# Performance work log

Hardware: AMD Instinct MI355X
Metric: run time of the kernel (lower is better)

The kernel has to match this reference:

```python
import jax, jax.numpy as jnp
import numpy as np

B, S, D, H = 2, 2048, 512, 8
DK = D // H
MASK_VALUE = -1e9


def setup_inputs() -> dict:
    key = jax.random.key(0)
    ks = jax.random.split(key, 12)
    scale = 1.0 / np.sqrt(D)
    inp = {
        "query": jax.random.normal(ks[0], (B, S, D), jnp.float32),
        "key": jax.random.normal(ks[1], (B, S, D), jnp.float32),
        "value": jax.random.normal(ks[2], (B, S, D), jnp.float32),
        # causal mask, broadcastable over batch and heads
        "mask": jnp.tril(jnp.ones((S, S), jnp.int32))[None, None, :, :],
        "Wq": jax.random.normal(ks[3], (D, D), jnp.float32) * scale,
        "bq": jax.random.normal(ks[4], (D,), jnp.float32) * scale,
        "Wk": jax.random.normal(ks[5], (D, D), jnp.float32) * scale,
        "bk": jax.random.normal(ks[6], (D,), jnp.float32) * scale,
        "Wv": jax.random.normal(ks[7], (D, D), jnp.float32) * scale,
        "bv": jax.random.normal(ks[8], (D,), jnp.float32) * scale,
        "Wo": jax.random.normal(ks[9], (D, D), jnp.float32) * scale,
        "bo": jax.random.normal(ks[10], (D,), jnp.float32) * scale,
    }
    return inp


def reference(query, key, value, mask, Wq, bq, Wk, bk, Wv, bv, Wo, bo):
    # linear projections (torch Linear: x @ W.T + b)
    q = query @ Wq.T + bq
    k = key @ Wk.T + bk
    v = value @ Wv.T + bv
    # split heads: [B,S,D] -> [B,H,S,DK]
    q = q.reshape(B, S, H, DK).transpose(0, 2, 1, 3)
    k = k.reshape(B, S, H, DK).transpose(0, 2, 1, 3)
    v = v.reshape(B, S, H, DK).transpose(0, 2, 1, 3)
    # scaled dot-product attention with explicit [B,H,S,S] score matrix
    scores = jnp.einsum("bhqd,bhkd->bhqk", q, k) / jnp.sqrt(jnp.float32(DK))
    scores = jnp.where(mask == 0, jnp.float32(MASK_VALUE), scores)
    attn = jax.nn.softmax(scores, axis=-1)
    x = jnp.einsum("bhqk,bhkd->bhqd", attn, v)
    # merge heads: [B,H,S,DK] -> [B,S,D]
    x = x.transpose(0, 2, 1, 3).reshape(B, S, D)
    return x @ Wo.T + bo
```

## Files before the change

### kernel.cpp

```cpp
#include <hip/hip_runtime.h>
#include <hip/hip_bf16.h>

#define B_   2
#define S_   2048
#define D_   512
#define H_   8
#define DK_  64
#define M_   (B_*S_)

typedef float  floatx4 __attribute__((ext_vector_type(4)));
typedef __bf16 bf16x8  __attribute__((ext_vector_type(8)));

#define MFMA16x16x32(a,b,c) __builtin_amdgcn_mfma_f32_16x16x32_bf16((a),(b),(c),0,0,0)

static __device__ __forceinline__ void load_lds16(const void* g, void* l) {
  __builtin_amdgcn_global_load_lds(
      (const __attribute__((address_space(1))) void*)g,
      (__attribute__((address_space(3))) void*)l,
      16, 0, 0);
}

static __device__ __forceinline__ bf16x8 cvt8(float4 a, float4 b) {
  bf16x8 r;
  r[0]=(__bf16)a.x; r[1]=(__bf16)a.y; r[2]=(__bf16)a.z; r[3]=(__bf16)a.w;
  r[4]=(__bf16)b.x; r[5]=(__bf16)b.y; r[6]=(__bf16)b.z; r[7]=(__bf16)b.w;
  return r;
}

static __device__ __forceinline__ int part_idx(int bh, int t, int s) {
  const int g = t >> 3;
  const int basec = (g == 2) ? 16 : ((g == 3) ? 40 : 0);
  return bh*72 + basec + (t - 8*g)*(g + 1) + s;
}

__global__ __launch_bounds__(256) void cvt_weights(
    const float* __restrict__ w0, const float* __restrict__ w1,
    const float* __restrict__ w2, const float* __restrict__ w3,
    __bf16* __restrict__ out)
{
  const int idx = (blockIdx.x * 256 + threadIdx.x) * 4;
  const float* src = (idx < 524288) ? ((idx < 262144) ? w0 : w1)
                                    : ((idx < 786432) ? w2 : w3);
  const int off = idx & 0x3FFFF;
  float4 v = *(const float4*)(src + off);
  __bf16* o = out + idx;
  o[0]=(__bf16)v.x; o[1]=(__bf16)v.y; o[2]=(__bf16)v.z; o[3]=(__bf16)v.w;
}


__global__ __launch_bounds__(256) void proj_qkv(
    const float* __restrict__ q_in, const float* __restrict__ k_in,
    const float* __restrict__ v_in, const __bf16* __restrict__ Wball,
    const float* __restrict__ bq, const float* __restrict__ bk, const float* __restrict__ bv,
    __bf16* __restrict__ Qb, __bf16* __restrict__ Kb, __bf16* __restrict__ Vtb)
{
  __shared__ __align__(16) __bf16 smem[12288];

  const int z = blockIdx.z;
  const float*  X32  = (z==0) ? q_in : (z==1) ? k_in : v_in;
  const __bf16* W    = Wball + (size_t)z * (D_*D_);
  const float*  bias = (z==0) ? bq : (z==1) ? bk : bv;

  const int m0 = blockIdx.x * 64;
  const int n0 = blockIdx.y * 128;
  const int tid  = threadIdx.x;
  const int w    = tid >> 6;
  const int lane = tid & 63;
  const int lcol = lane & 15;
  const int quad = lane >> 4;
  const int wm = w & 1, wn = w >> 1;

  const int au  = tid;
  const int arow = au >> 2, ac8 = (au & 3) * 8;
  const float* xsrc = X32 + (size_t)(m0 + arow)*D_ + ac8;

  floatx4 zero = {0.f,0.f,0.f,0.f};
  floatx4 acc[2][4];
#pragma unroll
  for (int i = 0; i < 2; ++i)
#pragma unroll
    for (int nt = 0; nt < 4; ++nt) acc[i][nt] = zero;

  auto stageB = [&](int bsel, int k0) {
#pragma unroll
    for (int j = 0; j < 2; ++j) {
      const int u = (j*4 + w)*64 + lane;
      load_lds16(W + (size_t)(n0 + (u >> 2))*D_ + k0 + (u & 3)*8,
                 (char*)(smem + 4096 + bsel*4096) + (j*4 + w)*1024);
    }
  };

  float4 f0, f1;
  stageB(0, 0);
  f0 = *(const float4*)(xsrc);
  f1 = *(const float4*)(xsrc + 4);
  *(bf16x8*)(smem + au*8) = cvt8(f0, f1);

  for (int it = 0; it < 16; ++it) {
    __syncthreads();
    const bool havenext = (it + 1 < 16);
    float4 g0, g1;
    if (havenext) {
      stageB((it+1)&1, (it+1)*32);
      g0 = *(const float4*)(xsrc + (it+1)*32);
      g1 = *(const float4*)(xsrc + (it+1)*32 + 4);
    }
    const __bf16* ab = smem + (it&1)*2048;
    const __bf16* bb = smem + 4096 + (it&1)*4096;
    bf16x8 af[2], bf[4];
#pragma unroll
    for (int i = 0; i < 2; ++i)
      af[i] = *(const bf16x8*)(ab + (wm*32 + i*16 + lcol)*32 + quad*8);
#pragma unroll
    for (int nt = 0; nt < 4; ++nt)
      bf[nt] = *(const bf16x8*)(bb + (wn*64 + nt*16 + lcol)*32 + quad*8);
#pragma unroll
    for (int i = 0; i < 2; ++i)
#pragma unroll
      for (int nt = 0; nt < 4; ++nt)
        acc[i][nt] = MFMA16x16x32(af[i], bf[nt], acc[i][nt]);
    if (havenext)
      *(bf16x8*)(smem + ((it+1)&1)*2048 + au*8) = cvt8(g0, g1);
  }

  __syncthreads();
#pragma unroll
  for (int nt = 0; nt < 4; ++nt) {
    const int n = n0 + wn*64 + nt*16 + lcol;
    const float bias_n = bias[n];
    const int h_l = (n >> 6) & 1;
    const int dk  = n & 63;
#pragma unroll
    for (int i = 0; i < 2; ++i)
#pragma unroll
      for (int r = 0; r < 4; ++r) {
        const int m = m0 + wm*32 + i*16 + quad*4 + r;
        const float val = acc[i][nt][r] + bias_n;
        const int klo = m & 63;
        int off;
        if (z == 0) {
          off = klo*64 + dk;
        } else if (z == 1) {
          off = (((klo>>4)*2 + (dk>>5))*64 + ((dk>>3)&3)*16 + (klo&15))*8 + (dk&7);
        } else {
          off = (((dk>>4)*2 + (klo>>5))*64 + ((klo>>3)&3)*16 + (dk&15))*8 + (klo&7);
        }
        smem[h_l*4096 + off] = (__bf16)val;
      }
  }
  __syncthreads();

  __bf16* dst = (z==0) ? Qb : (z==1) ? Kb : Vtb;
  const int bb2 = m0 >> 11;
  const int hh0 = n0 >> 6;
  const int cc0 = (m0 & 2047) >> 6;
#pragma unroll
  for (int it2 = 0; it2 < 4; ++it2) {
    const int u = it2*256 + tid;
    const int p = u >> 9, o = u & 511;
    const size_t base = ((size_t)(bb2*H_ + hh0 + p))*(S_*DK_) + (size_t)cc0*4096;
    *(bf16x8*)(dst + base + o*8) = *(const bf16x8*)(smem + p*4096 + o*8);
  }
}

__global__ __launch_bounds__(256) void attn_fwd(
    const __bf16* __restrict__ Qb, const __bf16* __restrict__ Kb,
    const __bf16* __restrict__ Vtb, __bf16* __restrict__ attnb,
    __bf16* __restrict__ Pb, float* __restrict__ Lb)
{
  __shared__ __align__(16) __bf16 kbuf[2][4096];
  __shared__ __align__(16) __bf16 vbuf[2][4096];
  __shared__ __align__(16) __bf16 pbuf[4][16*72];

  const int tid  = threadIdx.x;
  const int w    = tid >> 6;
  const int lane = tid & 63;
  const int lcol = lane & 15;
  const int quad = lane >> 4;
  const int hh = blockIdx.y;
  const int bb = blockIdx.z;

  const int wid = blockIdx.x;
  int t, s;
  if (wid < 8)       { t = wid;                  s = 0; }
  else if (wid < 24) { int u = wid - 8;  t = 8  + (u>>1); s = u & 1; }
  else if (wid < 48) { int u = wid - 24; int q3 = u/3; t = 16 + q3; s = u - 3*q3; }
  else               { int u = wid - 48; t = 24 + (u>>2); s = u & 3; }
  const bool single = (wid < 8);

  const int cbeg = s*8;
  const int cend = (cbeg + 8 < t + 1) ? (cbeg + 8) : (t + 1);
  const int q0  = t * 64;
  const int qr0 = q0 + w*16;

  const __bf16* Qp = Qb  + (size_t)(bb*H_ + hh) * S_ * DK_;
  const __bf16* Kp = Kb  + (size_t)(bb*H_ + hh) * S_ * DK_;
  const __bf16* Vp = Vtb + (size_t)(bb*H_ + hh) * DK_ * S_;

  const bf16x8 aq0 = *(const bf16x8*)(Qp + (size_t)(qr0 + lcol)*DK_ + quad*8);
  const bf16x8 aq1 = *(const bf16x8*)(Qp + (size_t)(qr0 + lcol)*DK_ + 32 + quad*8);

  floatx4 zero = {0.f,0.f,0.f,0.f};
  floatx4 acc[4] = {zero, zero, zero, zero};
  float lsum[4] = {0.f, 0.f, 0.f, 0.f};

  auto stage_chunk = [&](int bsel, int c) {
    const char* ksrc = (const char*)(Kp + (size_t)c * 4096);
    const char* vsrc = (const char*)(Vp + (size_t)c * 4096);
#pragma unroll
    for (int j = 0; j < 2; ++j) {
      const int off = w*2048 + j*1024;
      load_lds16(ksrc + off + lane*16, (char*)kbuf[bsel] + off);
      load_lds16(vsrc + off + lane*16, (char*)vbuf[bsel] + off);
    }
  };

  stage_chunk(0, cbeg);
  for (int c = cbeg; c < cend; ++c) {
    __syncthreads();
    if (c + 1 < cend) stage_chunk((c - cbeg + 1)&1, c+1);
    const int bsel = (c - cbeg) & 1;
    const int k0 = c * 64;
    const __bf16* kb = kbuf[bsel];
    const __bf16* vb = vbuf[bsel];

    floatx4 sc[4];
#pragma unroll
    for (int nt = 0; nt < 4; ++nt) {
      bf16x8 kf0 = *(const bf16x8*)(kb + (nt*2+0)*512 + lane*8);
      bf16x8 kf1 = *(const bf16x8*)(kb + (nt*2+1)*512 + lane*8);
      sc[nt] = MFMA16x16x32(aq1, kf1, MFMA16x16x32(aq0, kf0, zero));
    }

    const bool edge = (k0 + 63 > qr0);
#pragma unroll
    for (int nt = 0; nt < 4; ++nt) {
#pragma unroll
      for (int r = 0; r < 4; ++r) {
        float p = exp2f(sc[nt][r] * 0.18033688011112042f);
        if (edge) {
          const int qrow = qr0 + quad*4 + r;
          if (k0 + nt*16 + lcol > qrow) p = 0.f;
        }
        lsum[r] += p;
        pbuf[w][(quad*4 + r)*72 + nt*16 + lcol] = (__bf16)p;
      }
    }
    asm volatile("s_waitcnt lgkmcnt(0)" ::: "memory");

    const bf16x8 pa0 = *(const bf16x8*)(&pbuf[w][lcol*72 + quad*8]);
    const bf16x8 pa1 = *(const bf16x8*)(&pbuf[w][lcol*72 + 32 + quad*8]);
#pragma unroll
    for (int nt = 0; nt < 4; ++nt) {
      bf16x8 vf0 = *(const bf16x8*)(vb + (nt*2+0)*512 + lane*8);
      bf16x8 vf1 = *(const bf16x8*)(vb + (nt*2+1)*512 + lane*8);
      acc[nt] = MFMA16x16x32(pa0, vf0, acc[nt]);
      acc[nt] = MFMA16x16x32(pa1, vf1, acc[nt]);
    }
  }

  float tv[4];
#pragma unroll
  for (int r = 0; r < 4; ++r) {
    float v = lsum[r];
    v += __shfl_xor(v, 1, 16);
    v += __shfl_xor(v, 2, 16);
    v += __shfl_xor(v, 4, 16);
    v += __shfl_xor(v, 8, 16);
    tv[r] = v;
  }

  if (single) {
#pragma unroll
    for (int nt = 0; nt < 4; ++nt)
#pragma unroll
      for (int r = 0; r < 4; ++r) {
        const int q = qr0 + quad*4 + r;
        attnb[((size_t)(bb*S_ + q)) * D_ + hh*DK_ + nt*16 + lcol] =
            (__bf16)(acc[nt][r] / tv[r]);
      }
  } else {
    const int pidx = part_idx(bb*H_ + hh, t, s);

#pragma unroll
    for (int nt = 0; nt < 4; ++nt)
#pragma unroll
      for (int r = 0; r < 4; ++r)
        pbuf[w][(quad*4 + r)*72 + nt*16 + lcol] = (__bf16)acc[nt][r];
    asm volatile("s_waitcnt lgkmcnt(0)" ::: "memory");

    __bf16* pdst = Pb + (size_t)pidx*4096 + w*16*64;
#pragma unroll
    for (int i = 0; i < 2; ++i) {
      const int unit = i*64 + lane;
      const int row = unit >> 3, grp = unit & 7;
      *(bf16x8*)(pdst + row*64 + grp*8) =
          *(const bf16x8*)(&pbuf[w][row*72 + grp*8]);
    }
    if (lcol == 0) {
#pragma unroll
      for (int r = 0; r < 4; ++r)
        Lb[(size_t)pidx*64 + w*16 + quad*4 + r] = tv[r];
    }
  }
}

__global__ __launch_bounds__(256) void proj_out(
    const __bf16* __restrict__ attnb, const __bf16* __restrict__ Pb,
    const float* __restrict__ Lb, const __bf16* __restrict__ Wob,
    const float* __restrict__ bo, float* __restrict__ out)
{
  __shared__ __align__(16) __bf16 smem[12288];

  const int m0 = blockIdx.x * 64;
  const int n0 = blockIdx.y * 128;
  const int tid  = threadIdx.x;
  const int w    = tid >> 6;
  const int lane = tid & 63;
  const int lcol = lane & 15;
  const int quad = lane >> 4;
  const int wm = w & 1, wn = w >> 1;

  const int bb  = m0 >> 11;
  const int t   = (m0 & 2047) >> 6;
  const bool direct = (t < 8);
  const int g = t >> 3;
  const int nseg = g + 1;

  const int au  = tid;
  const int arow = au >> 2;
  const int ac8l = (au & 3) * 8;

  floatx4 zero = {0.f,0.f,0.f,0.f};
  floatx4 acc[2][4];
#pragma unroll
  for (int i = 0; i < 2; ++i)
#pragma unroll
    for (int nt = 0; nt < 4; ++nt) acc[i][nt] = zero;

  auto stageB = [&](int bsel, int k0) {
#pragma unroll
    for (int j = 0; j < 2; ++j) {
      const int u = (j*4 + w)*64 + lane;
      load_lds16(Wob + (size_t)(n0 + (u >> 2))*D_ + k0 + (u & 3)*8,
                 (char*)(smem + 4096 + bsel*4096) + (j*4 + w)*1024);
    }
  };
  auto stageA_direct = [&](int bsel, int k0) {
    load_lds16(attnb + (size_t)(m0 + arow)*D_ + k0 + ac8l,
               (char*)(smem + bsel*2048) + w*1024);
  };

  bf16x8 pv[4];
  float  pl[4];
  auto loadA_part = [&](int k0) {
    const int hh = k0 >> 6;
    const int cblk = k0 & 63;
    const int pidx0 = part_idx(bb*H_ + hh, t, 0);
#pragma unroll 4
    for (int s2 = 0; s2 < 4; ++s2) {
      if (s2 < nseg) {
        pv[s2] = *(const bf16x8*)(Pb + (size_t)(pidx0 + s2)*4096
                                   + arow*64 + cblk + ac8l);
        pl[s2] = Lb[(size_t)(pidx0 + s2)*64 + arow];
      }
    }
  };
  auto storeA_part = [&](int bsel) {
    float sum[8] = {0,0,0,0,0,0,0,0};
    float l = 0.f;
#pragma unroll 4
    for (int s2 = 0; s2 < 4; ++s2) {
      if (s2 < nseg) {
#pragma unroll
        for (int j = 0; j < 8; ++j) sum[j] += (float)pv[s2][j];
        l += pl[s2];
      }
    }
    const float rinv = 1.0f / l;
    bf16x8 o;
#pragma unroll
    for (int j = 0; j < 8; ++j) o[j] = (__bf16)(sum[j] * rinv);
    *(bf16x8*)(smem + bsel*2048 + au*8) = o;
  };

  stageB(0, 0);
  if (direct) {
    stageA_direct(0, 0);
  } else {
    loadA_part(0);
    storeA_part(0);
  }

  for (int it = 0; it < 16; ++it) {
    __syncthreads();
    const bool havenext = (it + 1 < 16);
    if (havenext) {
      stageB((it+1)&1, (it+1)*32);
      if (direct) stageA_direct((it+1)&1, (it+1)*32);
      else        loadA_part((it+1)*32);
    }
    const __bf16* ab = smem + (it&1)*2048;
    const __bf16* bbp = smem + 4096 + (it&1)*4096;
    bf16x8 af[2], bf[4];
#pragma unroll
    for (int i = 0; i < 2; ++i)
      af[i] = *(const bf16x8*)(ab + (wm*32 + i*16 + lcol)*32 + quad*8);
#pragma unroll
    for (int nt = 0; nt < 4; ++nt)
      bf[nt] = *(const bf16x8*)(bbp + (wn*64 + nt*16 + lcol)*32 + quad*8);
#pragma unroll
    for (int i = 0; i < 2; ++i)
#pragma unroll
      for (int nt = 0; nt < 4; ++nt)
        acc[i][nt] = MFMA16x16x32(af[i], bf[nt], acc[i][nt]);
    if (havenext && !direct) storeA_part((it+1)&1);
  }

#pragma unroll
  for (int nt = 0; nt < 4; ++nt) {
    const int n = n0 + wn*64 + nt*16 + lcol;
    const float bias_n = bo[n];
#pragma unroll
    for (int i = 0; i < 2; ++i)
#pragma unroll
      for (int r = 0; r < 4; ++r) {
        const int m = m0 + wm*32 + i*16 + quad*4 + r;
        out[(size_t)m * D_ + n] = acc[i][nt][r] + bias_n;
      }
  }
}

extern "C" void kernel_launch(void* const* d_in, const int* in_sizes, int n_in,
                              void* d_out, int out_size, void* d_ws, size_t ws_size,
                              hipStream_t stream) {
  const float* q_in = (const float*)d_in[0];
  const float* k_in = (const float*)d_in[1];
  const float* v_in = (const float*)d_in[2];
  const float* Wq = (const float*)d_in[4];
  const float* bq = (const float*)d_in[5];
  const float* Wk = (const float*)d_in[6];
  const float* bk = (const float*)d_in[7];
  const float* Wv = (const float*)d_in[8];
  const float* bv = (const float*)d_in[9];
  const float* Wo = (const float*)d_in[10];
  const float* bo = (const float*)d_in[11];
  float* out = (float*)d_out;

  __bf16* ws    = (__bf16*)d_ws;
  __bf16* Qb    = ws;
  __bf16* Kb    = ws + 1*2097152;
  __bf16* Vtb   = ws + 2*2097152;
  __bf16* attnb = ws + 3*2097152;
  __bf16* Wb    = ws + 4*2097152;
  __bf16* Pb    = Wb + 4*262144;
  float*  Lb    = (float*)(Pb + 1152*4096);

  cvt_weights<<<dim3(1024), dim3(256), 0, stream>>>(Wq, Wk, Wv, Wo, Wb);

  proj_qkv<<<dim3(M_/64, D_/128, 3), dim3(256), 0, stream>>>(
      q_in, k_in, v_in, Wb, bq, bk, bv, Qb, Kb, Vtb);

  attn_fwd<<<dim3(80, H_, B_), dim3(256), 0, stream>>>(
      Qb, Kb, Vtb, attnb, Pb, Lb);

  proj_out<<<dim3(M_/64, D_/128), dim3(256), 0, stream>>>(
      attnb, Pb, Lb, Wb + 3*262144, bo, out);
}
```

Before: 166.5 us.

## Fuse weight fp32-to-bf16 conversion into GEMMs and enlarge QKV tile to 128x128

Drops the separate cvt_weights kernel. The projection kernels now load fp32 weights directly and convert them to bf16 in registers before writing to LDS, which removes one launch and the bf16 weight round trip through memory. proj_qkv also grows its M tile from 64 to 128, doubling accumulators per wave so each staged weight tile is reused more, at the cost of more registers, more LDS and fewer blocks. Weight staging now goes through registers instead of async global-to-LDS loads, and every block re-reads and re-converts the fp32 weights.

```diff
diff --git a/kernel.cpp b/kernel.cpp
--- a/kernel.cpp
+++ b/kernel.cpp
@@ -33,35 +33,24 @@
   return bh*72 + basec + (t - 8*g)*(g + 1) + s;
 }
 
-__global__ __launch_bounds__(256) void cvt_weights(
-    const float* __restrict__ w0, const float* __restrict__ w1,
-    const float* __restrict__ w2, const float* __restrict__ w3,
-    __bf16* __restrict__ out)
-{
-  const int idx = (blockIdx.x * 256 + threadIdx.x) * 4;
-  const float* src = (idx < 524288) ? ((idx < 262144) ? w0 : w1)
-                                    : ((idx < 786432) ? w2 : w3);
-  const int off = idx & 0x3FFFF;
-  float4 v = *(const float4*)(src + off);
-  __bf16* o = out + idx;
-  o[0]=(__bf16)v.x; o[1]=(__bf16)v.y; o[2]=(__bf16)v.z; o[3]=(__bf16)v.w;
-}
-
 
 __global__ __launch_bounds__(256) void proj_qkv(
     const float* __restrict__ q_in, const float* __restrict__ k_in,
-    const float* __restrict__ v_in, const __bf16* __restrict__ Wball,
-    const float* __restrict__ bq, const float* __restrict__ bk, const float* __restrict__ bv,
+    const float* __restrict__ v_in,
+    const float* __restrict__ Wq32, const float* __restrict__ Wk32,
+    const float* __restrict__ Wv32,
+    const float* __restrict__ bq, const float* __restrict__ bk,
+    const float* __restrict__ bv,
     __bf16* __restrict__ Qb, __bf16* __restrict__ Kb, __bf16* __restrict__ Vtb)
 {
-  __shared__ __align__(16) __bf16 smem[12288];
+  __shared__ __align__(16) __bf16 smem[16384];
 
   const int z = blockIdx.z;
-  const float*  X32  = (z==0) ? q_in : (z==1) ? k_in : v_in;
-  const __bf16* W    = Wball + (size_t)z * (D_*D_);
-  const float*  bias = (z==0) ? bq : (z==1) ? bk : bv;
-
-  const int m0 = blockIdx.x * 64;
+  const float* X   = (z==0) ? q_in : (z==1) ? k_in : v_in;
+  const float* W32 = (z==0) ? Wq32 : (z==1) ? Wk32 : Wv32;
+  const float* bias = (z==0) ? bq : (z==1) ? bk : bv;
+
+  const int m0 = blockIdx.x * 128;
   const int n0 = blockIdx.y * 128;
   const int tid  = threadIdx.x;
   const int w    = tid >> 6;
@@ -70,57 +59,53 @@
   const int quad = lane >> 4;
   const int wm = w & 1, wn = w >> 1;
 
-  const int au  = tid;
-  const int arow = au >> 2, ac8 = (au & 3) * 8;
-  const float* xsrc = X32 + (size_t)(m0 + arow)*D_ + ac8;
+  const int uA0 = tid, uA1 = tid + 256;
 
   floatx4 zero = {0.f,0.f,0.f,0.f};
-  floatx4 acc[2][4];
-#pragma unroll
-  for (int i = 0; i < 2; ++i)
+  floatx4 acc[4][4];
+#pragma unroll
+  for (int i = 0; i < 4; ++i)
 #pragma unroll
     for (int nt = 0; nt < 4; ++nt) acc[i][nt] = zero;
 
-  auto stageB = [&](int bsel, int k0) {
-#pragma unroll
-    for (int j = 0; j < 2; ++j) {
-      const int u = (j*4 + w)*64 + lane;
-      load_lds16(W + (size_t)(n0 + (u >> 2))*D_ + k0 + (u & 3)*8,
-                 (char*)(smem + 4096 + bsel*4096) + (j*4 + w)*1024);
-    }
-  };
-
-  float4 f0, f1;
-  stageB(0, 0);
-  f0 = *(const float4*)(xsrc);
-  f1 = *(const float4*)(xsrc + 4);
-  *(bf16x8*)(smem + au*8) = cvt8(f0, f1);
-
+  float4 a00,a01,a10,a11, b00,b01,b10,b11;
+  auto ldAB = [&](int k0) {
+    const float* pa0 = X   + (size_t)(m0 + (uA0 >> 2))*D_ + k0 + (uA0 & 3)*8;
+    const float* pa1 = X   + (size_t)(m0 + (uA1 >> 2))*D_ + k0 + (uA1 & 3)*8;
+    const float* pb0 = W32 + (size_t)(n0 + (uA0 >> 2))*D_ + k0 + (uA0 & 3)*8;
+    const float* pb1 = W32 + (size_t)(n0 + (uA1 >> 2))*D_ + k0 + (uA1 & 3)*8;
+    a00 = *(const float4*)pa0; a01 = *(const float4*)(pa0 + 4);
+    a10 = *(const float4*)pa1; a11 = *(const float4*)(pa1 + 4);
+    b00 = *(const float4*)pb0; b01 = *(const float4*)(pb0 + 4);
+    b10 = *(const float4*)pb1; b11 = *(const float4*)(pb1 + 4);
+  };
+  auto wrAB = [&](int bsel) {
+    *(bf16x8*)(smem + bsel*4096 + uA0*8)        = cvt8(a00, a01);
+    *(bf16x8*)(smem + bsel*4096 + uA1*8)        = cvt8(a10, a11);
+    *(bf16x8*)(smem + 8192 + bsel*4096 + uA0*8) = cvt8(b00, b01);
+    *(bf16x8*)(smem + 8192 + bsel*4096 + uA1*8) = cvt8(b10, b11);
+  };
+
+  ldAB(0); wrAB(0);
   for (int it = 0; it < 16; ++it) {
     __syncthreads();
     const bool havenext = (it + 1 < 16);
-    float4 g0, g1;
-    if (havenext) {
-      stageB((it+1)&1, (it+1)*32);
-      g0 = *(const float4*)(xsrc + (it+1)*32);
-      g1 = *(const float4*)(xsrc + (it+1)*32 + 4);
-    }
-    const __bf16* ab = smem + (it&1)*2048;
-    const __bf16* bb = smem + 4096 + (it&1)*4096;
-    bf16x8 af[2], bf[4];
-#pragma unroll
-    for (int i = 0; i < 2; ++i)
-      af[i] = *(const bf16x8*)(ab + (wm*32 + i*16 + lcol)*32 + quad*8);
+    if (havenext) ldAB((it+1)*32);
+    const __bf16* ab = smem + (it&1)*4096;
+    const __bf16* bb = smem + 8192 + (it&1)*4096;
+    bf16x8 af[4], bf[4];
+#pragma unroll
+    for (int i = 0; i < 4; ++i)
+      af[i] = *(const bf16x8*)(ab + (wm*64 + i*16 + lcol)*32 + quad*8);
 #pragma unroll
     for (int nt = 0; nt < 4; ++nt)
       bf[nt] = *(const bf16x8*)(bb + (wn*64 + nt*16 + lcol)*32 + quad*8);
 #pragma unroll
-    for (int i = 0; i < 2; ++i)
+    for (int i = 0; i < 4; ++i)
 #pragma unroll
       for (int nt = 0; nt < 4; ++nt)
         acc[i][nt] = MFMA16x16x32(af[i], bf[nt], acc[i][nt]);
-    if (havenext)
-      *(bf16x8*)(smem + ((it+1)&1)*2048 + au*8) = cvt8(g0, g1);
+    if (havenext) wrAB((it+1)&1);
   }
 
   __syncthreads();
@@ -131,11 +116,12 @@
     const int h_l = (n >> 6) & 1;
     const int dk  = n & 63;
 #pragma unroll
-    for (int i = 0; i < 2; ++i)
+    for (int i = 0; i < 4; ++i)
 #pragma unroll
       for (int r = 0; r < 4; ++r) {
-        const int m = m0 + wm*32 + i*16 + quad*4 + r;
+        const int m = m0 + wm*64 + i*16 + quad*4 + r;
         const float val = acc[i][nt][r] + bias_n;
+        const int p = h_l*2 + ((m >> 6) & 1);
         const int klo = m & 63;
         int off;
         if (z == 0) {
@@ -145,7 +131,7 @@
         } else {
           off = (((dk>>4)*2 + (klo>>5))*64 + ((klo>>3)&3)*16 + (dk&15))*8 + (klo&7);
         }
-        smem[h_l*4096 + off] = (__bf16)val;
+        smem[p*4096 + off] = (__bf16)val;
       }
   }
   __syncthreads();
@@ -155,10 +141,11 @@
   const int hh0 = n0 >> 6;
   const int cc0 = (m0 & 2047) >> 6;
 #pragma unroll
-  for (int it2 = 0; it2 < 4; ++it2) {
+  for (int it2 = 0; it2 < 8; ++it2) {
     const int u = it2*256 + tid;
     const int p = u >> 9, o = u & 511;
-    const size_t base = ((size_t)(bb2*H_ + hh0 + p))*(S_*DK_) + (size_t)cc0*4096;
+    const size_t base = ((size_t)(bb2*H_ + hh0 + (p>>1)))*(S_*DK_)
+                      + (size_t)(cc0 + (p&1))*4096;
     *(bf16x8*)(dst + base + o*8) = *(const bf16x8*)(smem + p*4096 + o*8);
   }
 }
@@ -281,7 +268,6 @@
       }
   } else {
     const int pidx = part_idx(bb*H_ + hh, t, s);
-
 #pragma unroll
     for (int nt = 0; nt < 4; ++nt)
 #pragma unroll
@@ -307,7 +293,7 @@
 
 __global__ __launch_bounds__(256) void proj_out(
     const __bf16* __restrict__ attnb, const __bf16* __restrict__ Pb,
-    const float* __restrict__ Lb, const __bf16* __restrict__ Wob,
+    const float* __restrict__ Lb, const float* __restrict__ Wo32,
     const float* __restrict__ bo, float* __restrict__ out)
 {
   __shared__ __align__(16) __bf16 smem[12288];
@@ -331,6 +317,8 @@
   const int arow = au >> 2;
   const int ac8l = (au & 3) * 8;
 
+  const int uB0 = tid, uB1 = tid + 256;
+
   floatx4 zero = {0.f,0.f,0.f,0.f};
   floatx4 acc[2][4];
 #pragma unroll
@@ -338,13 +326,16 @@
 #pragma unroll
     for (int nt = 0; nt < 4; ++nt) acc[i][nt] = zero;
 
-  auto stageB = [&](int bsel, int k0) {
-#pragma unroll
-    for (int j = 0; j < 2; ++j) {
-      const int u = (j*4 + w)*64 + lane;
-      load_lds16(Wob + (size_t)(n0 + (u >> 2))*D_ + k0 + (u & 3)*8,
-                 (char*)(smem + 4096 + bsel*4096) + (j*4 + w)*1024);
-    }
+  float4 wb00, wb01, wb10, wb11;
+  auto ldB = [&](int k0) {
+    const float* p0 = Wo32 + (size_t)(n0 + (uB0 >> 2))*D_ + k0 + (uB0 & 3)*8;
+    const float* p1 = Wo32 + (size_t)(n0 + (uB1 >> 2))*D_ + k0 + (uB1 & 3)*8;
+    wb00 = *(const float4*)p0; wb01 = *(const float4*)(p0 + 4);
+    wb10 = *(const float4*)p1; wb11 = *(const float4*)(p1 + 4);
+  };
+  auto wrB = [&](int bsel) {
+    *(bf16x8*)(smem + 4096 + bsel*4096 + uB0*8) = cvt8(wb00, wb01);
+    *(bf16x8*)(smem + 4096 + bsel*4096 + uB1*8) = cvt8(wb10, wb11);
   };
   auto stageA_direct = [&](int bsel, int k0) {
     load_lds16(attnb + (size_t)(m0 + arow)*D_ + k0 + ac8l,
@@ -384,7 +375,7 @@
     *(bf16x8*)(smem + bsel*2048 + au*8) = o;
   };
 
-  stageB(0, 0);
+  ldB(0); wrB(0);
   if (direct) {
     stageA_direct(0, 0);
   } else {
@@ -396,7 +387,7 @@
     __syncthreads();
     const bool havenext = (it + 1 < 16);
     if (havenext) {
-      stageB((it+1)&1, (it+1)*32);
+      ldB((it+1)*32);
       if (direct) stageA_direct((it+1)&1, (it+1)*32);
       else        loadA_part((it+1)*32);
     }
@@ -414,7 +405,10 @@
 #pragma unroll
       for (int nt = 0; nt < 4; ++nt)
         acc[i][nt] = MFMA16x16x32(af[i], bf[nt], acc[i][nt]);
-    if (havenext && !direct) storeA_part((it+1)&1);
+    if (havenext) {
+      wrB((it+1)&1);
+      if (!direct) storeA_part((it+1)&1);
+    }
   }
 
 #pragma unroll
@@ -452,18 +446,15 @@
   __bf16* Kb    = ws + 1*2097152;
   __bf16* Vtb   = ws + 2*2097152;
   __bf16* attnb = ws + 3*2097152;
-  __bf16* Wb    = ws + 4*2097152;
-  __bf16* Pb    = Wb + 4*262144;
+  __bf16* Pb    = ws + 4*2097152;
   float*  Lb    = (float*)(Pb + 1152*4096);
 
-  cvt_weights<<<dim3(1024), dim3(256), 0, stream>>>(Wq, Wk, Wv, Wo, Wb);
-
-  proj_qkv<<<dim3(M_/64, D_/128, 3), dim3(256), 0, stream>>>(
-      q_in, k_in, v_in, Wb, bq, bk, bv, Qb, Kb, Vtb);
+  proj_qkv<<<dim3(M_/128, D_/128, 3), dim3(256), 0, stream>>>(
+      q_in, k_in, v_in, Wq, Wk, Wv, bq, bk, bv, Qb, Kb, Vtb);
 
   attn_fwd<<<dim3(80, H_, B_), dim3(256), 0, stream>>>(
       Qb, Kb, Vtb, attnb, Pb, Lb);
 
   proj_out<<<dim3(M_/64, D_/128), dim3(256), 0, stream>>>(
-      attnb, Pb, Lb, Wb + 3*262144, bo, out);
-}
+      attnb, Pb, Lb, Wo, bo, out);
+}
```

Measured after the change: 168.3 us. About the same (+1.1%).
